# Kernel tuning notes

Hardware: AMD Instinct MI355X
Metric: run time of the kernel (lower is better)

The kernel has to match this reference:

```python
import jax, jax.numpy as jnp
import numpy as np

HEADS = 16
D_MODEL = 1024
HEAD_DIM = D_MODEL // HEADS


def setup_inputs() -> dict:
    key = jax.random.key(0)
    ks = jax.random.split(key, 11)
    B, S = 4, 2048
    scale_in = 1.0 / np.sqrt(HEAD_DIM)
    scale_out = 1.0 / np.sqrt(D_MODEL)
    return {
        "values": jax.random.normal(ks[0], (B, S, D_MODEL), dtype=jnp.float32),
        "keys": jax.random.normal(ks[1], (B, S, D_MODEL), dtype=jnp.float32),
        "query": jax.random.normal(ks[2], (B, S, D_MODEL), dtype=jnp.float32),
        "wq": jax.random.normal(ks[3], (HEAD_DIM, HEAD_DIM), dtype=jnp.float32) * scale_in,
        "bq": jax.random.normal(ks[4], (HEAD_DIM,), dtype=jnp.float32) * 0.01,
        "wk": jax.random.normal(ks[5], (HEAD_DIM, HEAD_DIM), dtype=jnp.float32) * scale_in,
        "bk": jax.random.normal(ks[6], (HEAD_DIM,), dtype=jnp.float32) * 0.01,
        "wv": jax.random.normal(ks[7], (HEAD_DIM, HEAD_DIM), dtype=jnp.float32) * scale_in,
        "bv": jax.random.normal(ks[8], (HEAD_DIM,), dtype=jnp.float32) * 0.01,
        "wo": jax.random.normal(ks[9], (D_MODEL, D_MODEL), dtype=jnp.float32) * scale_out,
        "bo": jax.random.normal(ks[10], (D_MODEL,), dtype=jnp.float32) * 0.01,
    }


def reference(values, keys, query, wq, bq, wk, bk, wv, bv, wo, bo):
    B, Sq = query.shape[0], query.shape[1]
    Sk, Sv = keys.shape[1], values.shape[1]
    # reshape to (n, s, h, d); per-head linear shares one [d,d] weight across heads
    v = values.reshape(B, Sv, HEADS, HEAD_DIM) @ wv.T + bv
    k = keys.reshape(B, Sk, HEADS, HEAD_DIM) @ wk.T + bk
    q = query.reshape(B, Sq, HEADS, HEAD_DIM) @ wq.T + bq
    # scores scaled by sqrt(d_model) (as in original, NOT sqrt(head_dim))
    energy = jnp.einsum("nqhd,nkhd->nhqk", q, k)
    attn = jax.nn.softmax(energy / jnp.sqrt(jnp.float32(D_MODEL)), axis=-1)
    out = jnp.einsum("nhqk,nkhd->nqhd", attn, v).reshape(B, Sq, D_MODEL)
    return out @ wo.T + bo
```

## Files before the change

kernel.cpp:

```cpp
#include <hip/hip_runtime.h>

typedef unsigned short u16;
typedef short  bfrag  __attribute__((ext_vector_type(8), may_alias));
typedef unsigned long long ull_a __attribute__((may_alias));
typedef int    int_a  __attribute__((may_alias));
typedef int    i4_a   __attribute__((ext_vector_type(4), may_alias));
typedef float  f4_a   __attribute__((ext_vector_type(4), may_alias));
typedef unsigned u32x2 __attribute__((ext_vector_type(2)));
typedef __attribute__((ext_vector_type(4)))  float facc4;
typedef __attribute__((ext_vector_type(16))) float facc16;

#define SEQ   2048
#define NHEAD 16
#define HD    64
#define DM    1024
#define BH    64
#define NTOK  8192
#define QSC   0.04508422f

#if defined(__has_builtin)
#if __has_builtin(__builtin_amdgcn_cvt_pk_bf16_f32)
#define HAS_CVT_PK 1
#endif
#if __has_builtin(__builtin_amdgcn_permlane32_swap)
#define HAS_PLSWAP 1
#endif
#endif
#ifndef HAS_CVT_PK
#define HAS_CVT_PK 0
#endif
#ifndef HAS_PLSWAP
#define HAS_PLSWAP 0
#endif

__device__ __forceinline__ u16 f2bf(float f){
  union { float f; unsigned u; } x; x.f = f;
  unsigned r = x.u + 0x7FFFu + ((x.u >> 16) & 1u);
  return (u16)(r >> 16);
}
__device__ __forceinline__ unsigned pk2(float a, float b){
#if HAS_CVT_PK
  auto r = __builtin_amdgcn_cvt_pk_bf16_f32(a, b);
  union { decltype(r) v; unsigned u; } x; x.v = r; return x.u;
#else
  return (unsigned)f2bf(a) | ((unsigned)f2bf(b) << 16);
#endif
}
__device__ __forceinline__ unsigned long long pk4(float a, float b, float c, float d){
  return (unsigned long long)pk2(a,b) | ((unsigned long long)pk2(c,d) << 32);
}
__device__ __forceinline__ void swap32(unsigned &a, unsigned &b){
#if HAS_PLSWAP
  u32x2 r = __builtin_amdgcn_permlane32_swap(a, b, false, false);
  a = r[0]; b = r[1];
#else
  int lane = threadIdx.x & 63; int hh = lane >> 5;
  unsigned pa = (unsigned)__shfl_xor((int)a, 32, 64);
  unsigned pb = (unsigned)__shfl_xor((int)b, 32, 64);
  unsigned na = hh ? pb : a;
  unsigned nb = hh ? b  : pa;
  a = na; b = nb;
#endif
}
__device__ __forceinline__ bfrag ld8f(const float* p){
  f4_a a = *(const f4_a*)p;
  f4_a b = *(const f4_a*)(p + 4);
  union { bfrag v; unsigned u[4]; } r;
  r.u[0] = pk2(a[0],a[1]); r.u[1] = pk2(a[2],a[3]);
  r.u[2] = pk2(b[0],b[1]); r.u[3] = pk2(b[2],b[3]);
  return r.v;
}
__device__ __forceinline__ void stage16(const u16* g, u16* l){
  __builtin_amdgcn_global_load_lds((const __attribute__((address_space(1))) void*)g,
                                   (__attribute__((address_space(3))) void*)l, 16, 0, 0);
}

__global__ __launch_bounds__(256) void k_wconv(
  const float* __restrict__ wo, u16* __restrict__ dst)
{
  long i = ((long)blockIdx.x * 256 + threadIdx.x) * 8;
  f4_a a = *(const f4_a*)(wo + i);
  f4_a b = *(const f4_a*)(wo + i + 4);
  ull_a* p = (ull_a*)(dst + i);
  p[0] = pk4(a[0],a[1],a[2],a[3]);
  p[1] = pk4(b[0],b[1],b[2],b[3]);
}

__global__ __launch_bounds__(256, 4) void k_proj(
  const float* __restrict__ vin, const float* __restrict__ kin, const float* __restrict__ qin,
  const float* __restrict__ wq, const float* __restrict__ wk, const float* __restrict__ wv,
  const float* __restrict__ bq, const float* __restrict__ bk, const float* __restrict__ bv,
  u16* __restrict__ qo, u16* __restrict__ ko, u16* __restrict__ vt)
{
  __shared__ __align__(16) u16 LT[128*68];
  int tid = threadIdx.x;
  int wid = tid >> 6, lane = tid & 63;
  int ln = lane & 31, hh = lane >> 5;
  int h  = blockIdx.y;
  int t0 = blockIdx.x * 128;
  int b  = t0 >> 11;
  int s0 = t0 & 2047;
  int bh = b * NHEAD + h;
  int tok = t0 + wid*32 + ln;
  long xoff = (long)tok * DM + h * HD;

  auto run_mm = [&](const float* __restrict__ x, const float* __restrict__ w,
                    facc16* acc){
    bfrag bx[4], aw[2][4];
    #pragma unroll
    for (int ks = 0; ks < 4; ks++)
      bx[ks] = ld8f(x + xoff + ks*16 + hh*8);
    #pragma unroll
    for (int dt = 0; dt < 2; dt++)
      #pragma unroll
      for (int ks = 0; ks < 4; ks++)
        aw[dt][ks] = ld8f(w + (dt*32 + ln)*HD + ks*16 + hh*8);
    #pragma unroll
    for (int dt = 0; dt < 2; dt++){
      facc16 a;
      #pragma unroll
      for (int r = 0; r < 16; r++) a[r] = 0.f;
      #pragma unroll
      for (int ks = 0; ks < 4; ks++)
        a = __builtin_amdgcn_mfma_f32_32x32x16_bf16(aw[dt][ks], bx[ks], a, 0,0,0);
      acc[dt] = a;
    }
  };

  {
    facc16 acc[2]; run_mm(vin, wv, acc);
    int s = s0 + wid*32 + ln;
    long vb = (long)bh * HD * SEQ + s;
    #pragma unroll
    for (int dt = 0; dt < 2; dt++)
      #pragma unroll
      for (int g = 0; g < 4; g++){
        f4_a bb = *(const f4_a*)(bv + dt*32 + g*8 + 4*hh);
        #pragma unroll
        for (int j = 0; j < 4; j++){
          int d = dt*32 + g*8 + 4*hh + j;
          vt[vb + (long)d * SEQ] = f2bf(acc[dt][g*4+j] + bb[j]);
        }
      }
  }

  {
    facc16 acc[2]; run_mm(qin, wq, acc);
    int row = wid*32 + ln;
    #pragma unroll
    for (int dt = 0; dt < 2; dt++)
      #pragma unroll
      for (int g = 0; g < 4; g++){
        f4_a bb = *(const f4_a*)(bq + dt*32 + g*8 + 4*hh);
        *(ull_a*)&LT[row*68 + dt*32 + g*8 + 4*hh] =
          pk4((acc[dt][g*4+0]+bb[0])*QSC, (acc[dt][g*4+1]+bb[1])*QSC,
              (acc[dt][g*4+2]+bb[2])*QSC, (acc[dt][g*4+3]+bb[3])*QSC);
      }
  }
  __syncthreads();
  {
    int rr = tid >> 1, half = tid & 1;
    long gb = ((long)bh * SEQ + s0 + rr) * HD + half*32;
    #pragma unroll
    for (int j = 0; j < 4; j++)
      *(i4_a*)(qo + gb + j*8) = *(const i4_a*)&LT[rr*68 + half*32 + j*8];
  }
  __syncthreads();

  {
    facc16 acc[2]; run_mm(kin, wk, acc);
    int row = wid*32 + ln;
    #pragma unroll
    for (int dt = 0; dt < 2; dt++)
      #pragma unroll
      for (int g = 0; g < 4; g++){
        f4_a bb = *(const f4_a*)(bk + dt*32 + g*8 + 4*hh);
        *(ull_a*)&LT[row*68 + dt*32 + g*8 + 4*hh] =
          pk4(acc[dt][g*4+0]+bb[0], acc[dt][g*4+1]+bb[1],
              acc[dt][g*4+2]+bb[2], acc[dt][g*4+3]+bb[3]);
      }
  }
  __syncthreads();
  {
    int rr = tid >> 1, half = tid & 1;
    long gb = ((long)bh * SEQ + s0 + rr) * HD + half*32;
    #pragma unroll
    for (int j = 0; j < 4; j++)
      *(i4_a*)(ko + gb + j*8) = *(const i4_a*)&LT[rr*68 + half*32 + j*8];
  }
}

__global__ __launch_bounds__(512, 4) void k_attn(
  const u16* __restrict__ qws, const u16* __restrict__ kws, const u16* __restrict__ vt,
  u16* __restrict__ aout)
{
  __shared__ __align__(16) u16 KV[2][2][64*64];
  int tid = threadIdx.x;
  int wid = tid >> 6, lane = tid & 63;
  int ln = lane & 31, hh = lane >> 5;
  int bid = blockIdx.x;
  int xcd = bid & 7, lix = bid >> 3;
  int bh = xcd * 8 + (lix >> 3);
  int q0 = (lix & 7) * 256 + wid * 32;
  long base = (long)bh * SEQ * HD;

  int srow   = lane >> 3;
  int schunk = (lane & 7) ^ srow;

  bfrag qf[4];
  #pragma unroll
  for (int ks = 0; ks < 4; ks++)
    qf[ks] = *(const bfrag*)(qws + base + (long)(q0 + ln)*HD + ks*16 + hh*8);

  facc16 OO0, OO1;
  #pragma unroll
  for (int r = 0; r < 16; r++){ OO0[r] = 0.f; OO1[r] = 0.f; }
  float l_ = 0.f;

  stage16(kws + base + (long)(wid*8 + srow)*HD + schunk*8,  &KV[0][0][wid*512]);
  stage16(vt  + base + (long)(wid*8 + srow)*SEQ + schunk*8, &KV[0][1][wid*512]);

  auto tile = [&](int buf, int kt){
    __syncthreads();
    if (kt + 1 < 32){
      int k0n = (kt + 1) * 64;
      stage16(kws + base + (long)(k0n + wid*8 + srow)*HD + schunk*8, &KV[buf^1][0][wid*512]);
      stage16(vt  + base + (long)(wid*8 + srow)*SEQ + k0n + schunk*8, &KV[buf^1][1][wid*512]);
    }

    facc16 E0, E1;
    #pragma unroll
    for (int r = 0; r < 16; r++){ E0[r] = 0.f; E1[r] = 0.f; }
    __builtin_amdgcn_s_setprio(1);
    #pragma unroll
    for (int ks = 0; ks < 4; ks++){
      int sw = ((2*ks + hh) ^ (ln & 7)) * 8;
      bfrag kf0 = *(const bfrag*)&KV[buf][0][ ln      *64 + sw];
      bfrag kf1 = *(const bfrag*)&KV[buf][0][(32 + ln)*64 + sw];
      E0 = __builtin_amdgcn_mfma_f32_32x32x16_bf16(kf0, qf[ks], E0, 0,0,0);
      E1 = __builtin_amdgcn_mfma_f32_32x32x16_bf16(kf1, qf[ks], E1, 0,0,0);
    }
    __builtin_amdgcn_s_setprio(0);

    float rs = 0.f;
    #pragma unroll
    for (int r = 0; r < 16; r++){
      float p0 = __builtin_amdgcn_exp2f(E0[r]);
      float p1 = __builtin_amdgcn_exp2f(E1[r]);
      E0[r] = p0; E1[r] = p1; rs += p0 + p1;
    }
    l_ += rs;

    bfrag pf[4];
    #pragma unroll
    for (int half = 0; half < 2; half++){
      const facc16& P = half ? E1 : E0;
      #pragma unroll
      for (int k2 = 0; k2 < 2; k2++){
        int rb = k2 * 8;
        unsigned A0 = pk2(P[rb+0], P[rb+1]);
        unsigned A1 = pk2(P[rb+2], P[rb+3]);
        unsigned B0 = pk2(P[rb+4], P[rb+5]);
        unsigned B1 = pk2(P[rb+6], P[rb+7]);
        swap32(A0, B0);
        swap32(A1, B1);
        union { bfrag v; unsigned u[4]; } t;
        t.u[0] = A0; t.u[1] = A1; t.u[2] = B0; t.u[3] = B1;
        pf[half*2 + k2] = t.v;
      }
    }

    __builtin_amdgcn_s_setprio(1);
    #pragma unroll
    for (int ks = 0; ks < 4; ks++){
      int sw = ((2*ks + hh) ^ (ln & 7)) * 8;
      bfrag vf0 = *(const bfrag*)&KV[buf][1][ ln      *64 + sw];
      bfrag vf1 = *(const bfrag*)&KV[buf][1][(32 + ln)*64 + sw];
      OO0 = __builtin_amdgcn_mfma_f32_32x32x16_bf16(vf0, pf[ks], OO0, 0,0,0);
      OO1 = __builtin_amdgcn_mfma_f32_32x32x16_bf16(vf1, pf[ks], OO1, 0,0,0);
    }
    __builtin_amdgcn_s_setprio(0);
  };

  for (int kt = 0; kt < 32; kt += 2){
    tile(0, kt);
    tile(1, kt + 1);
  }

  l_ += __shfl_xor(l_, 32, 64);
  float inv = 1.0f / l_;
  int b_ = bh >> 4, h_ = bh & 15;
  long orow = ((long)(b_ * SEQ + q0 + ln) * NHEAD + h_) * HD;
  #pragma unroll
  for (int g = 0; g < 4; g++){
    *(ull_a*)(aout + orow +      8*g + 4*hh) =
      pk4(OO0[4*g]*inv, OO0[4*g+1]*inv, OO0[4*g+2]*inv, OO0[4*g+3]*inv);
    *(ull_a*)(aout + orow + 32 + 8*g + 4*hh) =
      pk4(OO1[4*g]*inv, OO1[4*g+1]*inv, OO1[4*g+2]*inv, OO1[4*g+3]*inv);
  }
}

__global__ __launch_bounds__(256, 2) void k_oproj(
  const u16* __restrict__ A, const u16* __restrict__ Bw,
  const float* __restrict__ bo, float* __restrict__ out)
{
  __shared__ __align__(16) u16 As[2][128*64];
  __shared__ __align__(16) u16 Bs[2][128*64];
  int tid  = threadIdx.x;
  int wid  = tid >> 6, lane = tid & 63;
  int quad = lane >> 4, col = lane & 15;
  int bid = blockIdx.x;
  int xcd = bid & 7, lix = bid >> 3;
  int m0 = (xcd * 8 + (lix >> 3)) * 128;
  int n0 = (lix & 7) * 128;
  int wm = (wid & 1) * 64, wn = (wid >> 1) * 64;

  facc4 acc[4][4];
  #pragma unroll
  for (int i = 0; i < 4; i++)
    #pragma unroll
    for (int j = 0; j < 4; j++) acc[i][j] = {0.f,0.f,0.f,0.f};

  int srow   = lane >> 3;
  int schunk = (lane & 7) ^ srow;
  const u16* Ag = A  + (long)(m0 + wid*8 + srow) * DM + schunk*8;
  const u16* Bg = Bw + (long)(n0 + wid*8 + srow) * DM + schunk*8;

  #pragma unroll
  for (int j = 0; j < 4; j++){
    stage16(Ag + (long)j*32*DM, &As[0][(j*32 + wid*8)*64]);
    stage16(Bg + (long)j*32*DM, &Bs[0][(j*32 + wid*8)*64]);
  }

  auto kstep = [&](int buf, int kt){
    __syncthreads();
    if (kt + 1 < 16){
      long k0 = (long)(kt + 1) * 64;
      #pragma unroll
      for (int j = 0; j < 4; j++){
        stage16(Ag + (long)j*32*DM + k0, &As[buf^1][(j*32 + wid*8)*64]);
        stage16(Bg + (long)j*32*DM + k0, &Bs[buf^1][(j*32 + wid*8)*64]);
      }
    }
    #pragma unroll
    for (int ks = 0; ks < 2; ks++){
      bfrag af[4], bf[4];
      #pragma unroll
      for (int i = 0; i < 4; i++){
        int row = wm + i*16 + col;
        af[i] = *(const bfrag*)&As[buf][row*64 + ((ks*4 + quad) ^ (col & 7))*8];
      }
      #pragma unroll
      for (int i = 0; i < 4; i++){
        int row = wn + i*16 + col;
        bf[i] = *(const bfrag*)&Bs[buf][row*64 + ((ks*4 + quad) ^ (col & 7))*8];
      }
      #pragma unroll
      for (int i = 0; i < 4; i++)
        #pragma unroll
        for (int j = 0; j < 4; j++)
          acc[i][j] = __builtin_amdgcn_mfma_f32_16x16x32_bf16(af[i], bf[j], acc[i][j], 0,0,0);
    }
  };

  for (int kt = 0; kt < 16; kt += 2){
    kstep(0, kt);
    kstep(1, kt + 1);
  }

  #pragma unroll
  for (int j = 0; j < 4; j++){
    int n = n0 + wn + j*16 + col;
    float bias = bo[n];
    #pragma unroll
    for (int i = 0; i < 4; i++){
      long mrow = m0 + wm + i*16 + quad*4;
      #pragma unroll
      for (int r = 0; r < 4; r++)
        out[(mrow + r) * DM + n] = acc[i][j][r] + bias;
    }
  }
}

extern "C" void kernel_launch(void* const* d_in, const int* in_sizes, int n_in,
                              void* d_out, int out_size, void* d_ws, size_t ws_size,
                              hipStream_t stream)
{
  const float* values = (const float*)d_in[0];
  const float* keys   = (const float*)d_in[1];
  const float* query  = (const float*)d_in[2];
  const float* wq = (const float*)d_in[3];
  const float* bq = (const float*)d_in[4];
  const float* wk = (const float*)d_in[5];
  const float* bk = (const float*)d_in[6];
  const float* wv = (const float*)d_in[7];
  const float* bv = (const float*)d_in[8];
  const float* wo = (const float*)d_in[9];
  const float* bo = (const float*)d_in[10];

  const long N = 8388608;
  u16* qws  = (u16*)d_ws;
  u16* kws  = qws  + N;
  u16* vws  = kws  + N;
  u16* vtws = vws  + N;
  u16* wob  = vtws + N;
  u16* aws  = vws;

  k_wconv <<<512,           256, 0, stream>>>(wo, wob);
  k_proj  <<<dim3(64, 16),  256, 0, stream>>>(values, keys, query, wq, wk, wv,
                                              bq, bk, bv, qws, kws, vtws);
  k_attn  <<<512,           512, 0, stream>>>(qws, kws, vtws, aws);
  k_oproj <<<512,           256, 0, stream>>>(aws, wob, bo, (float*)d_out);
}
```

Baseline: 285.2 us.

## Stage projection inputs via async LDS loads and pre-pack bf16 head weights

The head projection kernel now stages each 64-token fp32 input tile into swizzled LDS with global_load_lds. It no longer has each lane load fp32 rows directly. The small per-head weights are converted once to bf16 in MFMA-fragment order by the weight-conversion kernel, so each wave loads its A fragments with one vector load. The block tile shrinks to 64 tokens with four waves splitting tokens and output columns, doubling the grid, and the K-input staging overlaps the V/Q epilogues. This adds LDS traffic, extra barriers and a slightly larger conversion launch.

```diff
diff --git a/kernel.cpp b/kernel.cpp
--- a/kernel.cpp
+++ b/kernel.cpp
@@ -74,119 +74,143 @@
   __builtin_amdgcn_global_load_lds((const __attribute__((address_space(1))) void*)g,
                                    (__attribute__((address_space(3))) void*)l, 16, 0, 0);
 }
+__device__ __forceinline__ void stage16f(const float* g, float* l){
+  __builtin_amdgcn_global_load_lds((const __attribute__((address_space(1))) void*)g,
+                                   (__attribute__((address_space(3))) void*)l, 16, 0, 0);
+}
 
 __global__ __launch_bounds__(256) void k_wconv(
-  const float* __restrict__ wo, u16* __restrict__ dst)
+  const float* __restrict__ wo, const float* __restrict__ wq,
+  const float* __restrict__ wk, const float* __restrict__ wv,
+  u16* __restrict__ dst)
 {
   long i = ((long)blockIdx.x * 256 + threadIdx.x) * 8;
-  f4_a a = *(const f4_a*)(wo + i);
-  f4_a b = *(const f4_a*)(wo + i + 4);
-  ull_a* p = (ull_a*)(dst + i);
-  p[0] = pk4(a[0],a[1],a[2],a[3]);
-  p[1] = pk4(b[0],b[1],b[2],b[3]);
-}
-
-__global__ __launch_bounds__(256, 4) void k_proj(
+  if (i < 1048576){
+    f4_a a = *(const f4_a*)(wo + i);
+    f4_a b = *(const f4_a*)(wo + i + 4);
+    ull_a* p = (ull_a*)(dst + i);
+    p[0] = pk4(a[0],a[1],a[2],a[3]);
+    p[1] = pk4(b[0],b[1],b[2],b[3]);
+  } else {
+    long o = i - 1048576;
+    int m  = (int)(o >> 12);
+    int oo = (int)(o & 4095);
+    const float* src = (m == 0) ? wq : ((m == 1) ? wk : wv);
+    int lane = (oo >> 3) & 63, ks = (oo >> 9) & 3, dt = (oo >> 11);
+    int soff = (dt*32 + (lane & 31))*64 + ks*16 + (lane >> 5)*8;
+    f4_a a = *(const f4_a*)(src + soff);
+    f4_a b = *(const f4_a*)(src + soff + 4);
+    ull_a* p = (ull_a*)(dst + i);
+    p[0] = pk4(a[0],a[1],a[2],a[3]);
+    p[1] = pk4(b[0],b[1],b[2],b[3]);
+  }
+}
+
+__global__ __launch_bounds__(256) void k_proj(
   const float* __restrict__ vin, const float* __restrict__ kin, const float* __restrict__ qin,
-  const float* __restrict__ wq, const float* __restrict__ wk, const float* __restrict__ wv,
+  const u16* __restrict__ wqb, const u16* __restrict__ wkb, const u16* __restrict__ wvb,
   const float* __restrict__ bq, const float* __restrict__ bk, const float* __restrict__ bv,
   u16* __restrict__ qo, u16* __restrict__ ko, u16* __restrict__ vt)
 {
-  __shared__ __align__(16) u16 LT[128*68];
+  __shared__ __align__(16) float Xs[2][64*64];
+  __shared__ __align__(16) u16 LTq[64*68], LTk[64*68];
   int tid = threadIdx.x;
   int wid = tid >> 6, lane = tid & 63;
   int ln = lane & 31, hh = lane >> 5;
+  int tt = wid & 1, dt = wid >> 1;
   int h  = blockIdx.y;
-  int t0 = blockIdx.x * 128;
-  int b  = t0 >> 11;
-  int s0 = t0 & 2047;
+  int t0 = blockIdx.x * 64;
+  int b  = t0 >> 11, s0 = t0 & 2047;
   int bh = b * NHEAD + h;
-  int tok = t0 + wid*32 + ln;
-  long xoff = (long)tok * DM + h * HD;
-
-  auto run_mm = [&](const float* __restrict__ x, const float* __restrict__ w,
-                    facc16* acc){
-    bfrag bx[4], aw[2][4];
-    #pragma unroll
-    for (int ks = 0; ks < 4; ks++)
-      bx[ks] = ld8f(x + xoff + ks*16 + hh*8);
-    #pragma unroll
-    for (int dt = 0; dt < 2; dt++)
-      #pragma unroll
-      for (int ks = 0; ks < 4; ks++)
-        aw[dt][ks] = ld8f(w + (dt*32 + ln)*HD + ks*16 + hh*8);
-    #pragma unroll
-    for (int dt = 0; dt < 2; dt++){
-      facc16 a;
-      #pragma unroll
-      for (int r = 0; r < 16; r++) a[r] = 0.f;
-      #pragma unroll
-      for (int ks = 0; ks < 4; ks++)
-        a = __builtin_amdgcn_mfma_f32_32x32x16_bf16(aw[dt][ks], bx[ks], a, 0,0,0);
-      acc[dt] = a;
+
+  auto stage_mat = [&](const float* __restrict__ x, int buf){
+    #pragma unroll
+    for (int j = 0; j < 4; j++){
+      int g  = wid*4 + j;
+      int rl = g*4 + (lane >> 4);
+      int cg = (lane & 15) ^ (rl & 15);
+      stage16f(x + (long)(t0 + rl)*DM + h*HD + cg*4, &Xs[buf][g*4*64]);
     }
   };
+  auto bfr = [&](int buf, int ks){
+    int r  = tt*32 + ln;
+    int c0 = ks*4 + hh*2;
+    const f4_a* base = (const f4_a*)&Xs[buf][r*64];
+    f4_a a = base[ c0      ^ (r & 15)];
+    f4_a b = base[(c0 + 1) ^ (r & 15)];
+    union { bfrag v; unsigned u[4]; } rr;
+    rr.u[0] = pk2(a[0],a[1]); rr.u[1] = pk2(a[2],a[3]);
+    rr.u[2] = pk2(b[0],b[1]); rr.u[3] = pk2(b[2],b[3]);
+    return rr.v;
+  };
+  auto mm = [&](const u16* __restrict__ wb, int buf){
+    facc16 a;
+    #pragma unroll
+    for (int r = 0; r < 16; r++) a[r] = 0.f;
+    #pragma unroll
+    for (int ks = 0; ks < 4; ks++){
+      bfrag aw = *(const bfrag*)(wb + ((dt*4 + ks)*64 + lane)*8);
+      a = __builtin_amdgcn_mfma_f32_32x32x16_bf16(aw, bfr(buf, ks), a, 0,0,0);
+    }
+    return a;
+  };
+
+  stage_mat(vin, 0);
+  stage_mat(qin, 1);
+  __syncthreads();
 
   {
-    facc16 acc[2]; run_mm(vin, wv, acc);
-    int s = s0 + wid*32 + ln;
+    facc16 acc = mm(wvb, 0);
+    int s = s0 + tt*32 + ln;
     long vb = (long)bh * HD * SEQ + s;
     #pragma unroll
-    for (int dt = 0; dt < 2; dt++)
-      #pragma unroll
-      for (int g = 0; g < 4; g++){
-        f4_a bb = *(const f4_a*)(bv + dt*32 + g*8 + 4*hh);
-        #pragma unroll
-        for (int j = 0; j < 4; j++){
-          int d = dt*32 + g*8 + 4*hh + j;
-          vt[vb + (long)d * SEQ] = f2bf(acc[dt][g*4+j] + bb[j]);
-        }
-      }
-  }
+    for (int g = 0; g < 4; g++){
+      f4_a bb = *(const f4_a*)(bv + dt*32 + g*8 + 4*hh);
+      #pragma unroll
+      for (int j = 0; j < 4; j++)
+        vt[vb + (long)(dt*32 + g*8 + 4*hh + j) * SEQ] = f2bf(acc[g*4+j] + bb[j]);
+    }
+  }
+  __syncthreads();
+  stage_mat(kin, 0);
 
   {
-    facc16 acc[2]; run_mm(qin, wq, acc);
-    int row = wid*32 + ln;
-    #pragma unroll
-    for (int dt = 0; dt < 2; dt++)
-      #pragma unroll
-      for (int g = 0; g < 4; g++){
-        f4_a bb = *(const f4_a*)(bq + dt*32 + g*8 + 4*hh);
-        *(ull_a*)&LT[row*68 + dt*32 + g*8 + 4*hh] =
-          pk4((acc[dt][g*4+0]+bb[0])*QSC, (acc[dt][g*4+1]+bb[1])*QSC,
-              (acc[dt][g*4+2]+bb[2])*QSC, (acc[dt][g*4+3]+bb[3])*QSC);
-      }
+    facc16 acc = mm(wqb, 1);
+    int row = tt*32 + ln;
+    #pragma unroll
+    for (int g = 0; g < 4; g++){
+      f4_a bb = *(const f4_a*)(bq + dt*32 + g*8 + 4*hh);
+      *(ull_a*)&LTq[row*68 + dt*32 + g*8 + 4*hh] =
+        pk4((acc[g*4+0]+bb[0])*QSC, (acc[g*4+1]+bb[1])*QSC,
+            (acc[g*4+2]+bb[2])*QSC, (acc[g*4+3]+bb[3])*QSC);
+    }
+  }
+  __syncthreads();
+
+  {
+    int rr = tid >> 2, q4 = tid & 3;
+    long gb = ((long)bh * SEQ + s0 + rr) * HD + q4*16;
+    *(i4_a*)(qo + gb)     = *(const i4_a*)&LTq[rr*68 + q4*16];
+    *(i4_a*)(qo + gb + 8) = *(const i4_a*)&LTq[rr*68 + q4*16 + 8];
+  }
+
+  {
+    facc16 acc = mm(wkb, 0);
+    int row = tt*32 + ln;
+    #pragma unroll
+    for (int g = 0; g < 4; g++){
+      f4_a bb = *(const f4_a*)(bk + dt*32 + g*8 + 4*hh);
+      *(ull_a*)&LTk[row*68 + dt*32 + g*8 + 4*hh] =
+        pk4(acc[g*4+0]+bb[0], acc[g*4+1]+bb[1],
+            acc[g*4+2]+bb[2], acc[g*4+3]+bb[3]);
+    }
   }
   __syncthreads();
   {
-    int rr = tid >> 1, half = tid & 1;
-    long gb = ((long)bh * SEQ + s0 + rr) * HD + half*32;
-    #pragma unroll
-    for (int j = 0; j < 4; j++)
-      *(i4_a*)(qo + gb + j*8) = *(const i4_a*)&LT[rr*68 + half*32 + j*8];
-  }
-  __syncthreads();
-
-  {
-    facc16 acc[2]; run_mm(kin, wk, acc);
-    int row = wid*32 + ln;
-    #pragma unroll
-    for (int dt = 0; dt < 2; dt++)
-      #pragma unroll
-      for (int g = 0; g < 4; g++){
-        f4_a bb = *(const f4_a*)(bk + dt*32 + g*8 + 4*hh);
-        *(ull_a*)&LT[row*68 + dt*32 + g*8 + 4*hh] =
-          pk4(acc[dt][g*4+0]+bb[0], acc[dt][g*4+1]+bb[1],
-              acc[dt][g*4+2]+bb[2], acc[dt][g*4+3]+bb[3]);
-      }
-  }
-  __syncthreads();
-  {
-    int rr = tid >> 1, half = tid & 1;
-    long gb = ((long)bh * SEQ + s0 + rr) * HD + half*32;
-    #pragma unroll
-    for (int j = 0; j < 4; j++)
-      *(i4_a*)(ko + gb + j*8) = *(const i4_a*)&LT[rr*68 + half*32 + j*8];
+    int rr = tid >> 2, q4 = tid & 3;
+    long gb = ((long)bh * SEQ + s0 + rr) * HD + q4*16;
+    *(i4_a*)(ko + gb)     = *(const i4_a*)&LTk[rr*68 + q4*16];
+    *(i4_a*)(ko + gb + 8) = *(const i4_a*)&LTk[rr*68 + q4*16 + 8];
   }
 }
 
@@ -404,10 +428,13 @@
   u16* vws  = kws  + N;
   u16* vtws = vws  + N;
   u16* wob  = vtws + N;
+  u16* wqb  = wob + 1048576;
+  u16* wkb  = wqb + 4096;
+  u16* wvb  = wkb + 4096;
   u16* aws  = vws;
 
-  k_wconv <<<512,           256, 0, stream>>>(wo, wob);
-  k_proj  <<<dim3(64, 16),  256, 0, stream>>>(values, keys, query, wq, wk, wv,
+  k_wconv <<<518,           256, 0, stream>>>(wo, wq, wk, wv, wob);
+  k_proj  <<<dim3(128, 16), 256, 0, stream>>>(values, keys, query, wqb, wkb, wvb,
                                               bq, bk, bv, qws, kws, vtws);
   k_attn  <<<512,           512, 0, stream>>>(qws, kws, vtws, aws);
   k_oproj <<<512,           256, 0, stream>>>(aws, wob, bo, (float*)d_out);
```

Result: faster. 270.6 us (median of 2 runs) (-5.1%).
